# Kernel optimization log

Hardware: AMD Instinct MI355X
Metric: run time of the kernel (lower is better)

The kernel has to match this reference:

```python
import jax, jax.numpy as jnp
import numpy as np

N, E, IN, HID, HEADS, K = 50000, 800000, 7, 64, 4, 4


def _add_self_loops(src, dst, edge_attr, n):
    # PyG add_self_loops with fill_value='mean': loop attr = mean of incoming edge attrs per node
    ones = jnp.ones((src.shape[0],), edge_attr.dtype)
    cnt = jax.ops.segment_sum(ones, dst, num_segments=n)
    loop_attr = jax.ops.segment_sum(edge_attr, dst, num_segments=n) / jnp.maximum(cnt, 1.0)[:, None]
    ar = jnp.arange(n, dtype=src.dtype)
    return (jnp.concatenate([src, ar]), jnp.concatenate([dst, ar]),
            jnp.concatenate([edge_attr, loop_attr], axis=0))


def _gat_conv(x, src, dst, eattr, W, a_src, a_dst, We, a_edge, bias, heads, outc, concat, n):
    xw = (x @ W).reshape(n, heads, outc)                      # [N,H,C]
    al_s = jnp.sum(xw * a_src, -1)                            # [N,H]
    al_d = jnpm if False else jnp.sum(xw * a_dst, -1)         # [N,H]
    ew = (eattr @ We).reshape(-1, heads, outc)                # [E,H,C]
    al_e = jnp.sum(ew * a_edge, -1)                           # [E,H]
    alpha = jax.nn.leaky_relu(al_s[src] + al_d[dst] + al_e, 0.2)
    # segment softmax over incoming edges of each dst node (every node has a self loop)
    m = jax.ops.segment_max(alpha, dst, num_segments=n)
    alpha = jnp.exp(alpha - m[dst])
    denom = jax.ops.segment_sum(alpha, dst, num_segments=n)
    alpha = alpha / (denom[dst] + 1e-16)
    out = jax.ops.segment_sum(xw[src] * alpha[..., None], dst, num_segments=n)  # [N,H,C]
    out = out.reshape(n, heads * outc) if concat else out.mean(axis=1)
    return out + bias


def setup_inputs() -> dict:
    key = jax.random.key(0)
    ks = jax.random.split(key, 24)
    s = lambda d: 1.0 / np.sqrt(d)
    inp = {
        'x': jax.random.uniform(ks[0], (N, IN), jnp.float32),
        'edge_index': jax.random.randint(ks[1], (2, E), 0, N),
        'edge_attr': jax.random.uniform(ks[2], (E, 1), jnp.float32),
        'assignments': jax.random.randint(ks[3], (N,), 0, K),
        # conv1 (heads=4, concat)
        'W1': jax.random.normal(ks[4], (IN, HEADS * HID), jnp.float32) * s(IN),
        'att_src1': jax.random.normal(ks[5], (HEADS, HID), jnp.float32) * s(HID),
        'att_dst1': jax.random.normal(ks[6], (HEADS, HID), jnp.float32) * s(HID),
        'We1': jax.random.normal(ks[7], (1, HEADS * HID), jnp.float32),
        'att_e1': jax.random.normal(ks[8], (HEADS, HID), jnp.float32) * s(HID),
        'b1': jnp.zeros((HEADS * HID,), jnp.float32),
        # conv2 (heads=1, mean)
        'W2': jax.random.normal(ks[9], (HEADS * HID, HID), jnp.float32) * s(HEADS * HID),
        'att_src2': jax.random.normal(ks[10], (1, HID), jnp.float32) * s(HID),
        'att_dst2': jax.random.normal(ks[11], (1, HID), jnp.float32) * s(HID),
        'We2': jax.random.normal(ks[12], (1, HID), jnp.float32),
        'att_e2': jax.random.normal(ks[13], (1, HID), jnp.float32) * s(HID),
        'b2': jnp.zeros((HID,), jnp.float32),
        # actor MLP: Linear(HID+1, HID) -> ReLU -> Linear(HID, 1)
        'A1': jax.random.normal(ks[14], (HID + 1, HID), jnp.float32) * s(HID + 1),
        'c1': jnp.zeros((HID,), jnp.float32),
        'A2': jax.random.normal(ks[15], (HID, 1), jnp.float32) * s(HID),
        'c2': jnp.zeros((1,), jnp.float32),
    }
    return inp


def reference(x, edge_index, edge_attr, assignments,
              W1, att_src1, att_dst1, We1, att_e1, b1,
              W2, att_src2, att_dst2, We2, att_e2, b2,
              A1, c1, A2, c2):
    n = x.shape[0]
    src, dst, ea = _add_self_loops(edge_index[0], edge_index[1], edge_attr, n)
    h = jax.nn.elu(_gat_conv(x, src, dst, ea, W1, att_src1, att_dst1, We1, att_e1, b1,
                             HEADS, HID, True, n))
    h = _gat_conv(h, src, dst, ea, W2, att_src2, att_dst2, We2, att_e2, b2,
                  1, HID, False, n)
    # masked segment-mean pooling over clusters (all K clusters non-empty w.h.p.)
    ones = jnp.ones((n,), h.dtype)
    cnt = jax.ops.segment_sum(ones, assignments, num_segments=K)
    safe = jnp.maximum(cnt, 1.0)
    z = jax.ops.segment_sum(h, assignments, num_segments=K) / safe[:, None]     # [K,HID]
    cf = jax.ops.segment_sum(x[:, 6], assignments, num_segments=K) / safe       # [K]
    nonempty = (cnt > 0)
    z = jnp.where(nonempty[:, None], z, 0.0)
    cf = jnp.where(nonempty, cf, 0.0)
    zcf = jnp.concatenate([z, cf[:, None]], axis=-1)                            # [K,HID+1]
    logits = (jax.nn.relu(zcf @ A1 + c1) @ A2 + c2)[:, 0]                        # [K]
    probs = jax.nn.softmax(logits)[None, :]                                      # [1,K]
    z_flat = z.reshape(1, -1)                                                    # [1,K*HID]
    return probs, z_flat
```

## Files before the change

kernel.cpp:

```cpp
#include <hip/hip_runtime.h>
#include <hip/hip_bf16.h>

#define HEADS 4
#define KCL 4
#define BSHIFT 7
#define BW 128
#define NBUCKMAX 400
#define BCAP 2560
#define EPT 8
typedef unsigned long long u64;
typedef short short8 __attribute__((ext_vector_type(8)));
typedef float f32x4 __attribute__((ext_vector_type(4)));

__device__ __forceinline__ unsigned short bf16_rne(float f) {
    unsigned int u = __float_as_uint(f);
    u += 0x7FFFu + ((u >> 16) & 1u);
    return (unsigned short)(u >> 16);
}
__device__ __forceinline__ float bf16_to_f32(unsigned short h) {
    return __uint_as_float(((unsigned int)h) << 16);
}


__global__ __launch_bounds__(256) void k_prep_bin(const float* __restrict__ x,
                                                  const float* __restrict__ W1, const float* __restrict__ W2,
                                                  const float* __restrict__ as1, const float* __restrict__ ad1,
                                                  const float* __restrict__ as2, const float* __restrict__ ad2,
                                                  const float* __restrict__ We1, const float* __restrict__ ae1,
                                                  const float* __restrict__ We2, const float* __restrict__ ae2,
                                                  float* __restrict__ ce1, float* __restrict__ ce2,
                                                  float* __restrict__ u_s, float* __restrict__ u_d,
                                                  unsigned short* __restrict__ W2T,
                                                  float* __restrict__ nrec,
                                                  const int* __restrict__ src, const int* __restrict__ dst,
                                                  const float* __restrict__ ea,
                                                  unsigned int* __restrict__ gtail,
                                                  u64* __restrict__ gbuck,
                                                  int N_, int E_, int NB, int nbuck) {
    int t = threadIdx.x;
    if ((int)blockIdx.x >= NB) {
        __shared__ unsigned int cnt[NBUCKMAX];
        __shared__ unsigned int gb[NBUCKMAX];
        for (int i = t; i < nbuck; i += 256) cnt[i] = 0u;
        __syncthreads();
        int bid = blockIdx.x - NB;
        int e0 = bid * (256 * EPT) + t;
        u64 pk[EPT]; int bk[EPT]; unsigned int ls[EPT];
#pragma unroll
        for (int i = 0; i < EPT; i++) {
            int e = e0 + i * 256;
            bool valid = e < E_;
            int s = 0, d = 0; float a = 0.0f;
            if (valid) { s = src[e]; d = dst[e]; a = ea[e]; }
            int b = d >> BSHIFT;
            int lo = d & (BW - 1);
            pk[i] = ((u64)__float_as_uint(a) << 32) | ((u64)(unsigned int)lo << 24) | (unsigned int)s;
            bk[i] = b;
            ls[i] = valid ? atomicAdd(&cnt[b], 1u) : 0u;
        }
        __syncthreads();
        for (int i = t; i < nbuck; i += 256)
            gb[i] = (cnt[i] > 0u) ? atomicAdd(&gtail[i], cnt[i]) : 0u;
        __syncthreads();
#pragma unroll
        for (int i = 0; i < EPT; i++) {
            if (e0 + i * 256 < E_) {
                unsigned int pos = gb[bk[i]] + ls[i];
                if (pos < BCAP) gbuck[(size_t)bk[i] * BCAP + pos] = pk[i];
            }
        }
        return;
    }
    __shared__ float Ps_l[7][4], Pd_l[7][4];
    int h = t >> 6, lane = t & 63;
    for (int i = 0; i < 7; i++) {
        float a = W1[i * 256 + t];
        float ps = a * as1[t];
        float pd = a * ad1[t];
        for (int off = 32; off; off >>= 1) {
            ps += __shfl_down(ps, off, 64);
            pd += __shfl_down(pd, off, 64);
        }
        if (lane == 0) { Ps_l[i][h] = ps; Pd_l[i][h] = pd; }
    }
    if (blockIdx.x == 0) {
        float p = We1[t] * ae1[t];
        for (int off = 32; off; off >>= 1) p += __shfl_down(p, off, 64);
        if (lane == 0) ce1[h] = p;
        if (t < 64) {
            float q = We2[t] * ae2[t];
            for (int off = 32; off; off >>= 1) q += __shfl_down(q, off, 64);
            if (t == 0) ce2[0] = q;
        }
        float us = 0.f, ud = 0.f;
        const float* wr = W2 + t * 64;
        for (int n = 0; n < 64; n++) { us += wr[n] * as2[n]; ud += wr[n] * ad2[n]; }
        u_s[t] = us; u_d[t] = ud;
    }
    int gidx = blockIdx.x * 256 + t;
    if (gidx < 16384) {
        int nn = gidx & 63, k = gidx >> 6;
        W2T[nn * 256 + k] = bf16_rne(W2[k * 64 + nn]);
    }
    __syncthreads();
    int n = gidx;
    if (n >= N_) return;
    float xv[7];
#pragma unroll
    for (int i = 0; i < 7; i++) xv[i] = x[n * 7 + i];
    float4 als = make_float4(0.f, 0.f, 0.f, 0.f);
    float4 ald = make_float4(0.f, 0.f, 0.f, 0.f);
#pragma unroll
    for (int i = 0; i < 7; i++) {
        als.x += xv[i] * Ps_l[i][0]; als.y += xv[i] * Ps_l[i][1];
        als.z += xv[i] * Ps_l[i][2]; als.w += xv[i] * Ps_l[i][3];
        ald.x += xv[i] * Pd_l[i][0]; ald.y += xv[i] * Pd_l[i][1];
        ald.z += xv[i] * Pd_l[i][2]; ald.w += xv[i] * Pd_l[i][3];
    }
    float4* nr = (float4*)(nrec + (size_t)n * 16);
    nr[0] = als;
    nr[1] = ald;
    nr[2] = make_float4(xv[0], xv[1], xv[2], xv[3]);
    nr[3] = make_float4(xv[4], xv[5], xv[6], 0.0f);
}

__global__ __launch_bounds__(256) void k_scatter2(const unsigned int* __restrict__ gtail,
                                                  const u64* __restrict__ gbuck,
                                                  u64* __restrict__ gpacked,
                                                  int2* __restrict__ idx2, int N_) {
    __shared__ unsigned int rcnt[256], pre[256], cur[256];
    int b = blockIdx.x, t = threadIdx.x;
    unsigned int n = gtail[b]; if (n > BCAP) n = BCAP;
    int r0 = b << BSHIFT;
    rcnt[t] = 0u;
    __syncthreads();
    size_t base = (size_t)b * BCAP;
    for (unsigned int pos = t; pos < n; pos += 256) {
        u64 p = gbuck[base + pos];
        int lo = (int)((p >> 24) & 0xFFu);
        atomicAdd(&rcnt[lo], 1u);
    }
    __syncthreads();
    unsigned int v = rcnt[t];
    pre[t] = v;
    __syncthreads();
    for (int off = 1; off < 256; off <<= 1) {
        unsigned int u = (t >= off) ? pre[t - off] : 0u;
        __syncthreads();
        pre[t] += u;
        __syncthreads();
    }
    unsigned int excl = pre[t] - v;
    cur[t] = excl;
    if (t < BW && r0 + t < N_) idx2[r0 + t] = make_int2((int)(base + excl), (int)v);
    __syncthreads();
    for (unsigned int pos = t; pos < n; pos += 256) {
        u64 p = gbuck[base + pos];
        int lo = (int)((p >> 24) & 0xFFu);
        unsigned int slot = atomicAdd(&cur[lo], 1u);
        gpacked[base + slot] = p;
    }
}

__global__ __launch_bounds__(256) void k_agg1_xw2g(const int2* __restrict__ idx2,
                                                   const u64* __restrict__ gpacked,
                                                   const float* __restrict__ nrec,
                                                   const float* __restrict__ ce1,
                                                   const float* __restrict__ W1,
                                                   const float* __restrict__ b1,
                                                   const unsigned short* __restrict__ W2T,
                                                   const float* __restrict__ u_s,
                                                   const float* __restrict__ u_d,
                                                   unsigned short* __restrict__ xw2b,
                                                   float* __restrict__ al_s2,
                                                   float* __restrict__ al_d2, int N_) {
    __shared__ float Xs2[32][36];
    __shared__ __align__(16) unsigned short A_lds[32][264];
    __shared__ float als_p[32], ald_p[32];
    int t = threadIdx.x;
    int m0 = blockIdx.x * 32;
    {
        int dl = t >> 3, d = m0 + dl;
        int sub = t & 7, h = sub >> 1, half = sub & 1;
        bool act = d < N_;
        float4 A = make_float4(0.f, 0.f, 0.f, 0.f);
        float4 B = make_float4(0.f, 0.f, 0.f, 0.f);
        if (act) {
            int2 ix = idx2[d];
            const u64* row = gpacked + ix.x;
            int cnt = ix.y;
            const float* nd = nrec + (size_t)d * 16;
            float ald = nd[4 + h];
            float ce = ce1[h];
            float easum = 0.0f;
#define E1(J) { \
            u64 p = __builtin_nontemporal_load(&row[(J)]); \
            int s = (int)(p & 0xFFFFFFu); \
            float a = __uint_as_float((unsigned int)(p >> 32)); \
            const float* ns = nrec + (size_t)s * 16; \
            float als = ns[h]; \
            float4 xa = *(const float4*)(ns + 8); \
            float4 xb = *(const float4*)(ns + 12); \
            easum += a; \
            float v = als + ald + a * ce; \
            v = v > 0.f ? v : 0.2f * v; \
            float w = __expf(v); \
            A.x += w * xa.x; A.y += w * xa.y; A.z += w * xa.z; A.w += w * xa.w; \
            B.x += w * xb.x; B.y += w * xb.y; B.z += w * xb.z; B.w += w; }
            int j = half;
            for (; j + 6 < cnt; j += 8) { E1(j); E1(j + 2); E1(j + 4); E1(j + 6); }
            for (; j < cnt; j += 2) { E1(j); }
#undef E1
            A.x += __shfl_xor(A.x, 1, 64);
            A.y += __shfl_xor(A.y, 1, 64);
            A.z += __shfl_xor(A.z, 1, 64);
            A.w += __shfl_xor(A.w, 1, 64);
            B.x += __shfl_xor(B.x, 1, 64);
            B.y += __shfl_xor(B.y, 1, 64);
            B.z += __shfl_xor(B.z, 1, 64);
            B.w += __shfl_xor(B.w, 1, 64);
            easum += __shfl_xor(easum, 1, 64);
            if (!half) {
                float a_self = easum / fmaxf((float)cnt, 1.0f);
                float v = nd[h] + ald + a_self * ce;
                v = v > 0.f ? v : 0.2f * v;
                float w = __expf(v);
                float4 xa = *(const float4*)(nd + 8);
                float4 xb = *(const float4*)(nd + 12);
                A.x += w * xa.x; A.y += w * xa.y; A.z += w * xa.z; A.w += w * xa.w;
                B.x += w * xb.x; B.y += w * xb.y; B.z += w * xb.z; B.w += w;
            }
        }
        if (!half) {
            *(float4*)&Xs2[dl][h * 8] = A;
            *(float4*)&Xs2[dl][h * 8 + 4] = B;
        }
    }
    __syncthreads();
    {
        int r = t >> 3;
        int kk = t & 7;
        float ps = 0.f, pd = 0.f;
#pragma unroll
        for (int hh = 0; hh < 4; hh++) {
            float xv[7];
#pragma unroll
            for (int i = 0; i < 7; i++) xv[i] = Xs2[r][hh * 8 + i];
            float rw = 1.0f / (Xs2[r][hh * 8 + 7] + 1e-16f);
#pragma unroll
            for (int q = 0; q < 8; q++) {
                int k = hh * 64 + q * 8 + kk;
                float s = 0.f;
#pragma unroll
                for (int i = 0; i < 7; i++) s += xv[i] * W1[i * 256 + k];
                float v = s * rw + b1[k];
                float a = v > 0.f ? v : (__expf(v) - 1.0f);
                ps += a * u_s[k];
                pd += a * u_d[k];
                A_lds[r][k] = bf16_rne(a);
            }
        }
        ps += __shfl_xor(ps, 1, 64); pd += __shfl_xor(pd, 1, 64);
        ps += __shfl_xor(ps, 2, 64); pd += __shfl_xor(pd, 2, 64);
        ps += __shfl_xor(ps, 4, 64); pd += __shfl_xor(pd, 4, 64);
        if (kk == 0) { als_p[r] = ps; ald_p[r] = pd; }
    }
    __syncthreads();
    {
        int w = t >> 6, lane = t & 63;
        int mm = lane & 15, quad = lane >> 4;
        int n0 = w * 16;
        f32x4 acc0 = {0.f, 0.f, 0.f, 0.f};
        f32x4 acc1 = {0.f, 0.f, 0.f, 0.f};
        const unsigned short* bptr = W2T + (size_t)(n0 + mm) * 256;
#pragma unroll
        for (int step = 0; step < 8; step++) {
            int kf = step * 32 + quad * 8;
            short8 bf = *(const short8*)&bptr[kf];
            short8 af0 = *(const short8*)&A_lds[mm][kf];
            short8 af1 = *(const short8*)&A_lds[16 + mm][kf];
            acc0 = __builtin_amdgcn_mfma_f32_16x16x32_bf16(af0, bf, acc0, 0, 0, 0);
            acc1 = __builtin_amdgcn_mfma_f32_16x16x32_bf16(af1, bf, acc1, 0, 0, 0);
        }
#pragma unroll
        for (int r = 0; r < 4; r++) {
            int row0 = m0 + quad * 4 + r;
            if (row0 < N_) xw2b[(size_t)row0 * 64 + n0 + mm] = bf16_rne(acc0[r]);
            int row1 = row0 + 16;
            if (row1 < N_) xw2b[(size_t)row1 * 64 + n0 + mm] = bf16_rne(acc1[r]);
        }
    }
    if (t < 32 && m0 + t < N_) { al_s2[m0 + t] = als_p[t]; al_d2[m0 + t] = ald_p[t]; }
}

__global__ __launch_bounds__(256) void k_agg2f(const int2* __restrict__ idx2,
                                               const u64* __restrict__ gpacked,
                                               const float* __restrict__ al_s2,
                                               const float* __restrict__ al_d2,
                                               const float* __restrict__ ce2,
                                               const unsigned short* __restrict__ xw2b,
                                               float* __restrict__ h2, int N_) {
    int wid = threadIdx.x >> 6, lane = threadIdx.x & 63;
    int d = blockIdx.x * 4 + wid;
    if (d >= N_) return;
    int2 ix = idx2[d];
    const u64* row = gpacked + ix.x;
    int cnt = ix.y;
    float ald = al_d2[d];
    float ce = ce2[0];
    float acc = 0.0f;
    float wlane = 0.0f, alane = 0.0f;
    for (int pos = 0; pos < cnt; pos += 64) {
        int nle = min(64, cnt - pos);
        float w = 0.0f, a = 0.0f;
        int s = d;
        if (lane < nle) {
            u64 p = __builtin_nontemporal_load(&row[pos + lane]);
            s = (int)(p & 0xFFFFFFu);
            a = __uint_as_float((unsigned int)(p >> 32));
            float v = al_s2[s] + ald + a * ce;
            v = v > 0.f ? v : 0.2f * v;
            w = __expf(v);
        }
        wlane += w;
        alane += a;
        int jj = 0;
#define G1(OFS) \
        float w##OFS = __uint_as_float(__builtin_amdgcn_readlane(__float_as_uint(w), jj + OFS)); \
        int   s##OFS = __builtin_amdgcn_readlane(s, jj + OFS);
        for (; jj + 7 < nle; jj += 8) {
            G1(0) G1(1) G1(2) G1(3) G1(4) G1(5) G1(6) G1(7)
            acc += w0 * bf16_to_f32(xw2b[(size_t)s0 * 64 + lane])
                 + w1 * bf16_to_f32(xw2b[(size_t)s1 * 64 + lane])
                 + w2 * bf16_to_f32(xw2b[(size_t)s2 * 64 + lane])
                 + w3 * bf16_to_f32(xw2b[(size_t)s3 * 64 + lane])
                 + w4 * bf16_to_f32(xw2b[(size_t)s4 * 64 + lane])
                 + w5 * bf16_to_f32(xw2b[(size_t)s5 * 64 + lane])
                 + w6 * bf16_to_f32(xw2b[(size_t)s6 * 64 + lane])
                 + w7 * bf16_to_f32(xw2b[(size_t)s7 * 64 + lane]);
        }
        for (; jj < nle; jj++) {
            G1(0)
            acc += w0 * bf16_to_f32(xw2b[(size_t)s0 * 64 + lane]);
        }
#undef G1
    }
    float wsum = wlane, easum = alane;
    for (int off = 32; off; off >>= 1) {
        wsum += __shfl_xor(wsum, off, 64);
        easum += __shfl_xor(easum, off, 64);
    }
    float a_self = easum / fmaxf((float)cnt, 1.0f);
    float v = al_s2[d] + ald + a_self * ce;
    v = v > 0.f ? v : 0.2f * v;
    float w = __expf(v);
    acc += w * bf16_to_f32(xw2b[(size_t)d * 64 + lane]);
    wsum += w;
    h2[(size_t)d * 64 + lane] = acc / (wsum + 1e-16f);
}

__global__ __launch_bounds__(256) void k_pool(const float* __restrict__ h2, const float* __restrict__ x,
                                              const int* __restrict__ assign,
                                              float* __restrict__ zsum, float* __restrict__ cntK,
                                              float* __restrict__ cfK, int nNodes) {
    __shared__ float lz[KCL * 64];
    __shared__ float lc[KCL];
    __shared__ float lf[KCL];
    int t = threadIdx.x;
    lz[t] = 0.0f;
    if (t < KCL) { lc[t] = 0.0f; lf[t] = 0.0f; }
    __syncthreads();
    int lane = t & 63, wid = t >> 6;
    for (int n = blockIdx.x * 4 + wid; n < nNodes; n += gridDim.x * 4) {
        int a = assign[n];
        atomicAdd(&lz[a * 64 + lane], h2[(size_t)n * 64 + lane]);
        if (lane == 0) {
            atomicAdd(&lc[a], 1.0f);
            atomicAdd(&lf[a], x[n * 7 + 6]);
        }
    }
    __syncthreads();
    atomicAdd(&zsum[t], lz[t]);
    if (t < KCL) {
        atomicAdd(&cntK[t], lc[t]);
        atomicAdd(&cfK[t], lf[t]);
    }
}

__global__ __launch_bounds__(256) void k_head(const float* __restrict__ zsum, const float* __restrict__ cntK,
                                              const float* __restrict__ cfK, const float* __restrict__ b2,
                                              const float* __restrict__ A1, const float* __restrict__ c1,
                                              const float* __restrict__ A2, const float* __restrict__ c2,
                                              float* __restrict__ out) {
    __shared__ float zcf[KCL][65];
    __shared__ float logits[KCL];
    int t = threadIdx.x;
    int k = t >> 6, c = t & 63;
    float cn = cntK[k];
    float z = (cn > 0.f) ? (zsum[k * 64 + c] / fmaxf(cn, 1.0f) + b2[c]) : 0.0f;
    zcf[k][c] = z;
    out[4 + k * 64 + c] = z;
    if (c == 0) zcf[k][64] = (cn > 0.f) ? (cfK[k] / fmaxf(cn, 1.0f)) : 0.0f;
    __syncthreads();
    {
        int j = c;
        float acc = 0.0f;
        for (int i = 0; i < 65; i++) acc += zcf[k][i] * A1[i * 64 + j];
        float hr = fmaxf(acc + c1[j], 0.0f);
        float contrib = hr * A2[j];
        for (int off = 32; off; off >>= 1) contrib += __shfl_down(contrib, off, 64);
        if (j == 0) logits[k] = contrib + c2[0];
    }
    __syncthreads();
    if (t == 0) {
        float m = fmaxf(fmaxf(logits[0], logits[1]), fmaxf(logits[2], logits[3]));
        float e0 = expf(logits[0] - m), e1 = expf(logits[1] - m);
        float e2 = expf(logits[2] - m), e3 = expf(logits[3] - m);
        float s = e0 + e1 + e2 + e3;
        out[0] = e0 / s; out[1] = e1 / s; out[2] = e2 / s; out[3] = e3 / s;
    }
}

extern "C" void kernel_launch(void* const* d_in, const int* in_sizes, int n_in,
                              void* d_out, int out_size, void* d_ws, size_t ws_size,
                              hipStream_t stream) {
    const float* x      = (const float*)d_in[0];
    const int*   ei     = (const int*)d_in[1];
    const float* eattr  = (const float*)d_in[2];
    const int*   assign = (const int*)d_in[3];
    const float* W1     = (const float*)d_in[4];
    const float* as1    = (const float*)d_in[5];
    const float* ad1    = (const float*)d_in[6];
    const float* We1    = (const float*)d_in[7];
    const float* ae1    = (const float*)d_in[8];
    const float* b1     = (const float*)d_in[9];
    const float* W2     = (const float*)d_in[10];
    const float* as2    = (const float*)d_in[11];
    const float* ad2    = (const float*)d_in[12];
    const float* We2    = (const float*)d_in[13];
    const float* ae2    = (const float*)d_in[14];
    const float* b2     = (const float*)d_in[15];
    const float* A1     = (const float*)d_in[16];
    const float* c1     = (const float*)d_in[17];
    const float* A2     = (const float*)d_in[18];
    const float* c2     = (const float*)d_in[19];
    float* out = (float*)d_out;

    const int N_ = in_sizes[0] / 7;
    const int E_ = in_sizes[2];
    const int NB = (N_ + 255) / 256;
    const int nbuck = (N_ + BW - 1) >> BSHIFT;
    const int NBBIN = (E_ + 256 * EPT - 1) / (256 * EPT);
    const int* srcA = ei;
    const int* dstA = ei + E_;

    float* ws = (float*)d_ws;
    size_t Nz = (size_t)N_;
    float* nrec    = ws;
    float* al_s2   = nrec + 16 * Nz;
    float* al_d2   = al_s2 + Nz;
    float* ce1     = al_d2 + Nz;
    float* ce2     = ce1 + 4;
    float* zsum    = ce2 + 4;
    float* cntK    = zsum + 256;
    float* cfK     = cntK + 4;
    unsigned int* gtail = (unsigned int*)(cfK + 4);
    float* u_s     = (float*)(gtail + 392);
    float* u_d     = u_s + 256;
    unsigned short* xw2b = (unsigned short*)(u_d + 256);
    float* h2      = (float*)(xw2b + 64 * Nz);
    uintptr_t pp   = (uintptr_t)(h2 + 64 * Nz);
    u64* gbuck     = (u64*)((pp + 7) & ~(uintptr_t)7);
    u64* gpacked   = gbuck + (size_t)nbuck * BCAP;
    int2* idx2     = (int2*)(gpacked + (size_t)nbuck * BCAP);
    unsigned short* W2T = (unsigned short*)(idx2 + Nz);

    hipMemsetAsync(zsum, 0, (264 + 392) * sizeof(float), stream);

    k_prep_bin<<<NB + NBBIN, 256, 0, stream>>>(x, W1, W2, as1, ad1, as2, ad2,
                                               We1, ae1, We2, ae2,
                                               ce1, ce2, u_s, u_d, W2T, nrec,
                                               srcA, dstA, eattr, gtail, gbuck,
                                               N_, E_, NB, nbuck);

    k_scatter2<<<nbuck, 256, 0, stream>>>(gtail, gbuck, gpacked, idx2, N_);

    k_agg1_xw2g<<<(N_ + 31) / 32, 256, 0, stream>>>(idx2, gpacked, nrec, ce1,
                                                    W1, b1, W2T, u_s, u_d,
                                                    xw2b, al_s2, al_d2, N_);

    k_agg2f<<<(N_ + 3) / 4, 256, 0, stream>>>(idx2, gpacked, al_s2, al_d2, ce2, xw2b, h2, N_);
    k_pool<<<256, 256, 0, stream>>>(h2, x, assign, zsum, cntK, cfK, N_);

    k_head<<<1, 256, 0, stream>>>(zsum, cntK, cfK, b2, A1, c1, A2, c2, out);
}
```

Before: 240.7 us.

## Replace two-level bucket sort with per-node degree count, scan, and atomic scatter

Drops the bucketed binning (LDS-local counts, per-bucket global tails, and a second per-bucket counting-sort pass) and builds the CSR-by-destination directly. One pass counts degrees with global atomics, a wave-level scan assigns node offsets through an atomic cursor, and a scatter pass places each edge using a per-node atomic. This removes the intermediate bucket buffer and its extra read/write pass, and also the fixed bucket capacity that could silently drop edges. In exchange it uses many contended global atomics and adds a kernel launch. Node segments are no longer in node order, and edges within a segment land in nondeterministic order, which can change float summation order.

```diff
diff --git a/kernel.cpp b/kernel.cpp
--- a/kernel.cpp
+++ b/kernel.cpp
@@ -3,10 +3,6 @@
 
 #define HEADS 4
 #define KCL 4
-#define BSHIFT 7
-#define BW 128
-#define NBUCKMAX 400
-#define BCAP 2560
 #define EPT 8
 typedef unsigned long long u64;
 typedef short short8 __attribute__((ext_vector_type(8)));
@@ -22,7 +18,7 @@
 }
 
 
-__global__ __launch_bounds__(256) void k_prep_bin(const float* __restrict__ x,
+__global__ __launch_bounds__(256) void k_prep_cnt(const float* __restrict__ x,
                                                   const float* __restrict__ W1, const float* __restrict__ W2,
                                                   const float* __restrict__ as1, const float* __restrict__ ad1,
                                                   const float* __restrict__ as2, const float* __restrict__ ad2,
@@ -32,42 +28,16 @@
                                                   float* __restrict__ u_s, float* __restrict__ u_d,
                                                   unsigned short* __restrict__ W2T,
                                                   float* __restrict__ nrec,
-                                                  const int* __restrict__ src, const int* __restrict__ dst,
-                                                  const float* __restrict__ ea,
-                                                  unsigned int* __restrict__ gtail,
-                                                  u64* __restrict__ gbuck,
-                                                  int N_, int E_, int NB, int nbuck) {
+                                                  const int* __restrict__ dst,
+                                                  unsigned int* __restrict__ gdeg,
+                                                  int N_, int E_, int NB) {
     int t = threadIdx.x;
     if ((int)blockIdx.x >= NB) {
-        __shared__ unsigned int cnt[NBUCKMAX];
-        __shared__ unsigned int gb[NBUCKMAX];
-        for (int i = t; i < nbuck; i += 256) cnt[i] = 0u;
-        __syncthreads();
-        int bid = blockIdx.x - NB;
-        int e0 = bid * (256 * EPT) + t;
-        u64 pk[EPT]; int bk[EPT]; unsigned int ls[EPT];
+        int e0 = (blockIdx.x - NB) * (256 * EPT) + t;
 #pragma unroll
         for (int i = 0; i < EPT; i++) {
             int e = e0 + i * 256;
-            bool valid = e < E_;
-            int s = 0, d = 0; float a = 0.0f;
-            if (valid) { s = src[e]; d = dst[e]; a = ea[e]; }
-            int b = d >> BSHIFT;
-            int lo = d & (BW - 1);
-            pk[i] = ((u64)__float_as_uint(a) << 32) | ((u64)(unsigned int)lo << 24) | (unsigned int)s;
-            bk[i] = b;
-            ls[i] = valid ? atomicAdd(&cnt[b], 1u) : 0u;
-        }
-        __syncthreads();
-        for (int i = t; i < nbuck; i += 256)
-            gb[i] = (cnt[i] > 0u) ? atomicAdd(&gtail[i], cnt[i]) : 0u;
-        __syncthreads();
-#pragma unroll
-        for (int i = 0; i < EPT; i++) {
-            if (e0 + i * 256 < E_) {
-                unsigned int pos = gb[bk[i]] + ls[i];
-                if (pos < BCAP) gbuck[(size_t)bk[i] * BCAP + pos] = pk[i];
-            }
+            if (e < E_) atomicAdd(&gdeg[dst[e]], 1u);
         }
         return;
     }
@@ -124,41 +94,45 @@
     nr[3] = make_float4(xv[4], xv[5], xv[6], 0.0f);
 }
 
-__global__ __launch_bounds__(256) void k_scatter2(const unsigned int* __restrict__ gtail,
-                                                  const u64* __restrict__ gbuck,
-                                                  u64* __restrict__ gpacked,
-                                                  int2* __restrict__ idx2, int N_) {
-    __shared__ unsigned int rcnt[256], pre[256], cur[256];
-    int b = blockIdx.x, t = threadIdx.x;
-    unsigned int n = gtail[b]; if (n > BCAP) n = BCAP;
-    int r0 = b << BSHIFT;
-    rcnt[t] = 0u;
-    __syncthreads();
-    size_t base = (size_t)b * BCAP;
-    for (unsigned int pos = t; pos < n; pos += 256) {
-        u64 p = gbuck[base + pos];
-        int lo = (int)((p >> 24) & 0xFFu);
-        atomicAdd(&rcnt[lo], 1u);
-    }
-    __syncthreads();
-    unsigned int v = rcnt[t];
-    pre[t] = v;
-    __syncthreads();
-    for (int off = 1; off < 256; off <<= 1) {
-        unsigned int u = (t >= off) ? pre[t - off] : 0u;
-        __syncthreads();
-        pre[t] += u;
-        __syncthreads();
-    }
-    unsigned int excl = pre[t] - v;
-    cur[t] = excl;
-    if (t < BW && r0 + t < N_) idx2[r0 + t] = make_int2((int)(base + excl), (int)v);
-    __syncthreads();
-    for (unsigned int pos = t; pos < n; pos += 256) {
-        u64 p = gbuck[base + pos];
-        int lo = (int)((p >> 24) & 0xFFu);
-        unsigned int slot = atomicAdd(&cur[lo], 1u);
-        gpacked[base + slot] = p;
+__global__ __launch_bounds__(256) void k_offsets(const unsigned int* __restrict__ gdeg,
+                                                 unsigned int* __restrict__ cursor,
+                                                 int2* __restrict__ idx2,
+                                                 unsigned int* __restrict__ nodecur, int N_) {
+    int tid = blockIdx.x * 256 + threadIdx.x;
+    int lane = threadIdx.x & 63;
+    unsigned int deg = (tid < N_) ? gdeg[tid] : 0u;
+    unsigned int inc = deg;
+#pragma unroll
+    for (int off = 1; off < 64; off <<= 1) {
+        unsigned int u = __shfl_up(inc, off, 64);
+        if (lane >= off) inc += u;
+    }
+    unsigned int tot = __shfl(inc, 63, 64);
+    unsigned int base = 0u;
+    if (lane == 63) base = atomicAdd(cursor, tot);
+    base = __shfl(base, 63, 64);
+    unsigned int start = base + inc - deg;
+    if (tid < N_) {
+        idx2[tid] = make_int2((int)start, (int)deg);
+        nodecur[tid] = start;
+    }
+}
+
+__global__ __launch_bounds__(256) void k_scatter_d(const int* __restrict__ src, const int* __restrict__ dst,
+                                                   const float* __restrict__ ea,
+                                                   unsigned int* __restrict__ nodecur,
+                                                   u64* __restrict__ gpacked, int E_) {
+    int e0 = blockIdx.x * (256 * EPT) + threadIdx.x;
+#pragma unroll
+    for (int i = 0; i < EPT; i++) {
+        int e = e0 + i * 256;
+        if (e < E_) {
+            int s = src[e];
+            int d = dst[e];
+            float a = ea[e];
+            unsigned int pos = atomicAdd(&nodecur[d], 1u);
+            gpacked[pos] = ((u64)__float_as_uint(a) << 32) | (unsigned int)s;
+        }
     }
 }
 
@@ -449,7 +423,6 @@
     const int N_ = in_sizes[0] / 7;
     const int E_ = in_sizes[2];
     const int NB = (N_ + 255) / 256;
-    const int nbuck = (N_ + BW - 1) >> BSHIFT;
     const int NBBIN = (E_ + 256 * EPT - 1) / (256 * EPT);
     const int* srcA = ei;
     const int* dstA = ei + E_;
@@ -464,26 +437,28 @@
     float* zsum    = ce2 + 4;
     float* cntK    = zsum + 256;
     float* cfK     = cntK + 4;
-    unsigned int* gtail = (unsigned int*)(cfK + 4);
-    float* u_s     = (float*)(gtail + 392);
+    unsigned int* cursor = (unsigned int*)(cfK + 4);
+    unsigned int* gdeg   = cursor + 4;
+    float* u_s     = (float*)(gdeg + Nz);
     float* u_d     = u_s + 256;
     unsigned short* xw2b = (unsigned short*)(u_d + 256);
     float* h2      = (float*)(xw2b + 64 * Nz);
     uintptr_t pp   = (uintptr_t)(h2 + 64 * Nz);
-    u64* gbuck     = (u64*)((pp + 7) & ~(uintptr_t)7);
-    u64* gpacked   = gbuck + (size_t)nbuck * BCAP;
-    int2* idx2     = (int2*)(gpacked + (size_t)nbuck * BCAP);
-    unsigned short* W2T = (unsigned short*)(idx2 + Nz);
-
-    hipMemsetAsync(zsum, 0, (264 + 392) * sizeof(float), stream);
-
-    k_prep_bin<<<NB + NBBIN, 256, 0, stream>>>(x, W1, W2, as1, ad1, as2, ad2,
+    u64* gpacked   = (u64*)((pp + 7) & ~(uintptr_t)7);
+    int2* idx2     = (int2*)(gpacked + (size_t)E_);
+    unsigned int* nodecur = (unsigned int*)(idx2 + Nz);
+    unsigned short* W2T = (unsigned short*)(nodecur + Nz);
+
+    hipMemsetAsync(zsum, 0, (size_t)(268 + N_) * sizeof(float), stream);
+
+    k_prep_cnt<<<NB + NBBIN, 256, 0, stream>>>(x, W1, W2, as1, ad1, as2, ad2,
                                                We1, ae1, We2, ae2,
                                                ce1, ce2, u_s, u_d, W2T, nrec,
-                                               srcA, dstA, eattr, gtail, gbuck,
-                                               N_, E_, NB, nbuck);
-
-    k_scatter2<<<nbuck, 256, 0, stream>>>(gtail, gbuck, gpacked, idx2, N_);
+                                               dstA, gdeg, N_, E_, NB);
+
+    k_offsets<<<NB, 256, 0, stream>>>(gdeg, cursor, idx2, nodecur, N_);
+
+    k_scatter_d<<<NBBIN, 256, 0, stream>>>(srcA, dstA, eattr, nodecur, gpacked, E_);
 
     k_agg1_xw2g<<<(N_ + 31) / 32, 256, 0, stream>>>(idx2, gpacked, nrec, ce1,
                                                     W1, b1, W2T, u_s, u_d,
```

New measurement: 321.5 us. 1.34x slower.

## Compact CSR output with global degree counts and atomic cursor allocation

Applied to the files above, without the earlier changes.

Per-node in-degrees are now counted with global atomics during binning. The scatter kernel then uses a wave-shuffle prefix scan over those degrees and claims a contiguous range from a global cursor, which replaces the LDS histogram and the log-step shared-memory scan. The packed edge array becomes dense (E entries) instead of padded per bucket, which may improve locality for the aggregation kernels. In exchange it adds 800K global atomics on dst, a larger memset covering the degree array, and a bucket order that is no longer deterministic; bucket capacity is also raised.

```diff
diff --git a/kernel.cpp b/kernel.cpp
--- a/kernel.cpp
+++ b/kernel.cpp
@@ -6,7 +6,7 @@
 #define BSHIFT 7
 #define BW 128
 #define NBUCKMAX 400
-#define BCAP 2560
+#define BCAP 2816
 #define EPT 8
 typedef unsigned long long u64;
 typedef short short8 __attribute__((ext_vector_type(8)));
@@ -35,6 +35,7 @@
                                                   const int* __restrict__ src, const int* __restrict__ dst,
                                                   const float* __restrict__ ea,
                                                   unsigned int* __restrict__ gtail,
+                                                  unsigned int* __restrict__ gdeg,
                                                   u64* __restrict__ gbuck,
                                                   int N_, int E_, int NB, int nbuck) {
     int t = threadIdx.x;
@@ -57,6 +58,7 @@
             pk[i] = ((u64)__float_as_uint(a) << 32) | ((u64)(unsigned int)lo << 24) | (unsigned int)s;
             bk[i] = b;
             ls[i] = valid ? atomicAdd(&cnt[b], 1u) : 0u;
+            if (valid) atomicAdd(&gdeg[d], 1u);
         }
         __syncthreads();
         for (int i = t; i < nbuck; i += 256)
@@ -125,40 +127,45 @@
 }
 
 __global__ __launch_bounds__(256) void k_scatter2(const unsigned int* __restrict__ gtail,
+                                                  const unsigned int* __restrict__ gdeg,
+                                                  unsigned int* __restrict__ cursor,
                                                   const u64* __restrict__ gbuck,
                                                   u64* __restrict__ gpacked,
                                                   int2* __restrict__ idx2, int N_) {
-    __shared__ unsigned int rcnt[256], pre[256], cur[256];
+    __shared__ unsigned int cur[BW];
+    __shared__ unsigned int wtot[2];
+    __shared__ unsigned int sbase;
     int b = blockIdx.x, t = threadIdx.x;
     unsigned int n = gtail[b]; if (n > BCAP) n = BCAP;
     int r0 = b << BSHIFT;
-    rcnt[t] = 0u;
+    int lane = t & 63;
+    unsigned int deg = 0u, inc = 0u;
+    if (t < BW) {
+        int r = r0 + t;
+        deg = (r < N_) ? gdeg[r] : 0u;
+        inc = deg;
+#pragma unroll
+        for (int off = 1; off < 64; off <<= 1) {
+            unsigned int u = __shfl_up(inc, off, 64);
+            if (lane >= off) inc += u;
+        }
+        if (lane == 63) wtot[t >> 6] = inc;
+    }
+    __syncthreads();
+    if (t == 0) sbase = atomicAdd(cursor, wtot[0] + wtot[1]);
+    __syncthreads();
+    if (t < BW) {
+        unsigned int start = sbase + ((t >= 64) ? wtot[0] : 0u) + inc - deg;
+        cur[t] = start;
+        if (r0 + t < N_) idx2[r0 + t] = make_int2((int)start, (int)deg);
+    }
     __syncthreads();
     size_t base = (size_t)b * BCAP;
     for (unsigned int pos = t; pos < n; pos += 256) {
         u64 p = gbuck[base + pos];
         int lo = (int)((p >> 24) & 0xFFu);
-        atomicAdd(&rcnt[lo], 1u);
-    }
-    __syncthreads();
-    unsigned int v = rcnt[t];
-    pre[t] = v;
-    __syncthreads();
-    for (int off = 1; off < 256; off <<= 1) {
-        unsigned int u = (t >= off) ? pre[t - off] : 0u;
-        __syncthreads();
-        pre[t] += u;
-        __syncthreads();
-    }
-    unsigned int excl = pre[t] - v;
-    cur[t] = excl;
-    if (t < BW && r0 + t < N_) idx2[r0 + t] = make_int2((int)(base + excl), (int)v);
-    __syncthreads();
-    for (unsigned int pos = t; pos < n; pos += 256) {
-        u64 p = gbuck[base + pos];
-        int lo = (int)((p >> 24) & 0xFFu);
         unsigned int slot = atomicAdd(&cur[lo], 1u);
-        gpacked[base + slot] = p;
+        gpacked[slot] = p;
     }
 }
 
@@ -464,26 +471,28 @@
     float* zsum    = ce2 + 4;
     float* cntK    = zsum + 256;
     float* cfK     = cntK + 4;
-    unsigned int* gtail = (unsigned int*)(cfK + 4);
-    float* u_s     = (float*)(gtail + 392);
+    unsigned int* cursor = (unsigned int*)(cfK + 4);
+    unsigned int* gtail  = cursor + 4;
+    unsigned int* gdeg   = gtail + 400;
+    float* u_s     = (float*)(gdeg + Nz);
     float* u_d     = u_s + 256;
     unsigned short* xw2b = (unsigned short*)(u_d + 256);
     float* h2      = (float*)(xw2b + 64 * Nz);
     uintptr_t pp   = (uintptr_t)(h2 + 64 * Nz);
     u64* gbuck     = (u64*)((pp + 7) & ~(uintptr_t)7);
     u64* gpacked   = gbuck + (size_t)nbuck * BCAP;
-    int2* idx2     = (int2*)(gpacked + (size_t)nbuck * BCAP);
+    int2* idx2     = (int2*)(gpacked + (size_t)E_);
     unsigned short* W2T = (unsigned short*)(idx2 + Nz);
 
-    hipMemsetAsync(zsum, 0, (264 + 392) * sizeof(float), stream);
+    hipMemsetAsync(zsum, 0, (size_t)(668 + N_) * sizeof(float), stream);
 
     k_prep_bin<<<NB + NBBIN, 256, 0, stream>>>(x, W1, W2, as1, ad1, as2, ad2,
                                                We1, ae1, We2, ae2,
                                                ce1, ce2, u_s, u_d, W2T, nrec,
-                                               srcA, dstA, eattr, gtail, gbuck,
+                                               srcA, dstA, eattr, gtail, gdeg, gbuck,
                                                N_, E_, NB, nbuck);
 
-    k_scatter2<<<nbuck, 256, 0, stream>>>(gtail, gbuck, gpacked, idx2, N_);
+    k_scatter2<<<nbuck, 256, 0, stream>>>(gtail, gdeg, cursor, gbuck, gpacked, idx2, N_);
 
     k_agg1_xw2g<<<(N_ + 31) / 32, 256, 0, stream>>>(idx2, gpacked, nrec, ce1,
                                                     W1, b1, W2T, u_s, u_d,
```

Result: slower. 270.6 us (+12.4%).

## Fuse per-bucket edge sorting into first aggregation kernel with 32-node buckets

Applied to the files above, without the earlier changes.

Shrinks buckets from 128 to 32 destination nodes so that one bucket lines up with one aggregation block. The counting sort of each bucket now runs inside k_agg1_xw2g in shared memory, and the separate k_scatter2 launch is removed. Layer-1 aggregation reads the sorted edges from LDS instead of global memory, while gpacked and idx2 are still written out for layer 2. The costs are more binning buckets with a smaller capacity (1024 edges per bucket, so overflow truncation is a risk) and extra shared memory, which may lower occupancy.

```diff
diff --git a/kernel.cpp b/kernel.cpp
--- a/kernel.cpp
+++ b/kernel.cpp
@@ -3,10 +3,10 @@
 
 #define HEADS 4
 #define KCL 4
-#define BSHIFT 7
-#define BW 128
-#define NBUCKMAX 400
-#define BCAP 2560
+#define BSHIFT 5
+#define BW 32
+#define NBUCKMAX 1568
+#define BCAP 1024
 #define EPT 8
 typedef unsigned long long u64;
 typedef short short8 __attribute__((ext_vector_type(8)));
@@ -124,46 +124,10 @@
     nr[3] = make_float4(xv[4], xv[5], xv[6], 0.0f);
 }
 
-__global__ __launch_bounds__(256) void k_scatter2(const unsigned int* __restrict__ gtail,
-                                                  const u64* __restrict__ gbuck,
-                                                  u64* __restrict__ gpacked,
-                                                  int2* __restrict__ idx2, int N_) {
-    __shared__ unsigned int rcnt[256], pre[256], cur[256];
-    int b = blockIdx.x, t = threadIdx.x;
-    unsigned int n = gtail[b]; if (n > BCAP) n = BCAP;
-    int r0 = b << BSHIFT;
-    rcnt[t] = 0u;
-    __syncthreads();
-    size_t base = (size_t)b * BCAP;
-    for (unsigned int pos = t; pos < n; pos += 256) {
-        u64 p = gbuck[base + pos];
-        int lo = (int)((p >> 24) & 0xFFu);
-        atomicAdd(&rcnt[lo], 1u);
-    }
-    __syncthreads();
-    unsigned int v = rcnt[t];
-    pre[t] = v;
-    __syncthreads();
-    for (int off = 1; off < 256; off <<= 1) {
-        unsigned int u = (t >= off) ? pre[t - off] : 0u;
-        __syncthreads();
-        pre[t] += u;
-        __syncthreads();
-    }
-    unsigned int excl = pre[t] - v;
-    cur[t] = excl;
-    if (t < BW && r0 + t < N_) idx2[r0 + t] = make_int2((int)(base + excl), (int)v);
-    __syncthreads();
-    for (unsigned int pos = t; pos < n; pos += 256) {
-        u64 p = gbuck[base + pos];
-        int lo = (int)((p >> 24) & 0xFFu);
-        unsigned int slot = atomicAdd(&cur[lo], 1u);
-        gpacked[base + slot] = p;
-    }
-}
-
-__global__ __launch_bounds__(256) void k_agg1_xw2g(const int2* __restrict__ idx2,
-                                                   const u64* __restrict__ gpacked,
+__global__ __launch_bounds__(256) void k_agg1_xw2g(const unsigned int* __restrict__ gtail,
+                                                   const u64* __restrict__ gbuck,
+                                                   u64* __restrict__ gpacked,
+                                                   int2* __restrict__ idx2,
                                                    const float* __restrict__ nrec,
                                                    const float* __restrict__ ce1,
                                                    const float* __restrict__ W1,
@@ -176,9 +140,43 @@
                                                    float* __restrict__ al_d2, int N_) {
     __shared__ float Xs2[32][36];
     __shared__ __align__(16) unsigned short A_lds[32][264];
+    __shared__ u64 esorted[BCAP];
+    __shared__ unsigned int rdeg[32], rstart[32], rcur[32];
     __shared__ float als_p[32], ald_p[32];
     int t = threadIdx.x;
-    int m0 = blockIdx.x * 32;
+    int b = blockIdx.x;
+    int m0 = b * 32;
+    size_t base = (size_t)b * BCAP;
+    u64* raw = (u64*)&A_lds[0][0];
+    unsigned int n = gtail[b]; if (n > BCAP) n = BCAP;
+    if (t < 32) rdeg[t] = 0u;
+    __syncthreads();
+    for (unsigned int pos = t; pos < n; pos += 256) {
+        u64 p = __builtin_nontemporal_load(&gbuck[base + pos]);
+        raw[pos] = p;
+        atomicAdd(&rdeg[(unsigned int)(p >> 24) & 31u], 1u);
+    }
+    __syncthreads();
+    if (t < 32) {
+        unsigned int deg = rdeg[t];
+        unsigned int inc = deg;
+#pragma unroll
+        for (int off = 1; off < 32; off <<= 1) {
+            unsigned int u = __shfl_up(inc, off, 64);
+            if (t >= off) inc += u;
+        }
+        unsigned int start = inc - deg;
+        rstart[t] = start; rcur[t] = start;
+        if (m0 + t < N_) idx2[m0 + t] = make_int2((int)(base + start), (int)deg);
+    }
+    __syncthreads();
+    for (unsigned int pos = t; pos < n; pos += 256) {
+        u64 p = raw[pos];
+        unsigned int slot = atomicAdd(&rcur[(unsigned int)(p >> 24) & 31u], 1u);
+        esorted[slot] = p;
+    }
+    __syncthreads();
+    for (unsigned int pos = t; pos < n; pos += 256) gpacked[base + pos] = esorted[pos];
     {
         int dl = t >> 3, d = m0 + dl;
         int sub = t & 7, h = sub >> 1, half = sub & 1;
@@ -186,15 +184,14 @@
         float4 A = make_float4(0.f, 0.f, 0.f, 0.f);
         float4 B = make_float4(0.f, 0.f, 0.f, 0.f);
         if (act) {
-            int2 ix = idx2[d];
-            const u64* row = gpacked + ix.x;
-            int cnt = ix.y;
+            const u64* row = esorted + rstart[dl];
+            int cnt = (int)rdeg[dl];
             const float* nd = nrec + (size_t)d * 16;
             float ald = nd[4 + h];
             float ce = ce1[h];
             float easum = 0.0f;
 #define E1(J) { \
-            u64 p = __builtin_nontemporal_load(&row[(J)]); \
+            u64 p = row[(J)]; \
             int s = (int)(p & 0xFFFFFFu); \
             float a = __uint_as_float((unsigned int)(p >> 32)); \
             const float* ns = nrec + (size_t)s * 16; \
@@ -464,8 +461,8 @@
     float* zsum    = ce2 + 4;
     float* cntK    = zsum + 256;
     float* cfK     = cntK + 4;
-    unsigned int* gtail = (unsigned int*)(cfK + 4);
-    float* u_s     = (float*)(gtail + 392);
+    unsigned int* gtail  = (unsigned int*)(cfK + 4);
+    float* u_s     = (float*)(gtail + NBUCKMAX);
     float* u_d     = u_s + 256;
     unsigned short* xw2b = (unsigned short*)(u_d + 256);
     float* h2      = (float*)(xw2b + 64 * Nz);
@@ -475,7 +472,7 @@
     int2* idx2     = (int2*)(gpacked + (size_t)nbuck * BCAP);
     unsigned short* W2T = (unsigned short*)(idx2 + Nz);
 
-    hipMemsetAsync(zsum, 0, (264 + 392) * sizeof(float), stream);
+    hipMemsetAsync(zsum, 0, (size_t)(264 + NBUCKMAX) * sizeof(float), stream);
 
     k_prep_bin<<<NB + NBBIN, 256, 0, stream>>>(x, W1, W2, as1, ad1, as2, ad2,
                                                We1, ae1, We2, ae2,
@@ -483,11 +480,9 @@
                                                srcA, dstA, eattr, gtail, gbuck,
                                                N_, E_, NB, nbuck);
 
-    k_scatter2<<<nbuck, 256, 0, stream>>>(gtail, gbuck, gpacked, idx2, N_);
-
-    k_agg1_xw2g<<<(N_ + 31) / 32, 256, 0, stream>>>(idx2, gpacked, nrec, ce1,
-                                                    W1, b1, W2T, u_s, u_d,
-                                                    xw2b, al_s2, al_d2, N_);
+    k_agg1_xw2g<<<nbuck, 256, 0, stream>>>(gtail, gbuck, gpacked, idx2, nrec, ce1,
+                                           W1, b1, W2T, u_s, u_d,
+                                           xw2b, al_s2, al_d2, N_);
 
     k_agg2f<<<(N_ + 3) / 4, 256, 0, stream>>>(idx2, gpacked, al_s2, al_d2, ce2, xw2b, h2, N_);
     k_pool<<<256, 256, 0, stream>>>(h2, x, assign, zsum, cntK, cfK, N_);
```

Result: faster. 233.3 us (-3.1%).
